# Kernel optimization log

Measured on AMD Instinct MI355X. Metric: run time of the kernel, lower is better.

Reference implementation:

```python
import jax, jax.numpy as jnp
import numpy as np
from jax import lax

WIN = 8
SHIFT = 4
HEADS = 8
EPS = 1e-5

def _rel_pos_index(ws):
    coords = np.stack(np.meshgrid(np.arange(ws), np.arange(ws), indexing='ij'))  # (2,ws,ws)
    flat = coords.reshape(2, -1)
    rel = (flat[:, :, None] - flat[:, None, :]).transpose(1, 2, 0)
    rel[..., 0] += ws - 1
    rel[..., 1] += ws - 1
    rel[..., 0] *= 2 * ws - 1
    return rel.sum(-1)  # (ws*ws, ws*ws)

REL_IDX = _rel_pos_index(WIN)

def _attn_mask(H, W, ws, ss):
    # static shifted-window mask, values 0 / -100 like the torch code
    img = np.zeros((H, W))
    cnt = 0
    for h in (slice(0, -ws), slice(-ws, -ss), slice(-ss, None)):
        for w in (slice(0, -ws), slice(-ws, -ss), slice(-ss, None)):
            img[h, w] = cnt
            cnt += 1
    mw = img.reshape(H // ws, ws, W // ws, ws).transpose(0, 2, 1, 3).reshape(-1, ws * ws)
    diff = mw[:, None, :] - mw[:, :, None]  # [nW,1,N]-[nW,N,1]
    return jnp.asarray(np.where(diff != 0, -100.0, 0.0).astype(np.float32))

def _ln(x, w, b):
    m = x.mean(-1, keepdims=True)
    v = ((x - m) ** 2).mean(-1, keepdims=True)
    return (x - m) / jnp.sqrt(v + EPS) * w + b

def _win_part(x, ws):
    B, H, W, C = x.shape
    x = x.reshape(B, H // ws, ws, W // ws, ws, C).transpose(0, 1, 3, 2, 4, 5)
    return x.reshape(-1, ws * ws, C)

def _win_rev(w, ws, H, W, B):
    x = w.reshape(B, H // ws, W // ws, ws, ws, -1).transpose(0, 1, 3, 2, 4, 5)
    return x.reshape(B, H, W, -1)

def setup_inputs() -> dict:
    key = jax.random.key(0)
    ks = jax.random.split(key, 10)
    B, H, W, C, HID = 4, 128, 128, 256, 1024
    p = lambda i, shape: jax.random.normal(ks[i], shape, jnp.float32) * 0.02
    return dict(
        x=jax.random.normal(ks[0], (B, H * W, C), jnp.float32),
        H=H, W=W,
        norm1_w=jnp.ones((C,), jnp.float32), norm1_b=jnp.zeros((C,), jnp.float32),
        wq=p(1, (C, C)), bq=jnp.zeros((C,), jnp.float32),
        wkv=p(2, (C, 2 * C)), bkv=jnp.zeros((2 * C,), jnp.float32),
        rpb=p(3, ((2 * WIN - 1) ** 2, HEADS)),
        proj_w=p(4, (C, C)), proj_b=jnp.zeros((C,), jnp.float32),
        norm2_w=jnp.ones((C,), jnp.float32), norm2_b=jnp.zeros((C,), jnp.float32),
        lin1_w=p(5, (C, HID)), lin1_b=jnp.zeros((HID,), jnp.float32),
        dw_w=p(6, (HID, 1, 3, 3)), dw_b=jnp.zeros((HID,), jnp.float32),
        lin2_w=p(7, (HID, C)), lin2_b=jnp.zeros((C,), jnp.float32),
    )

def _forward(x, H, W, norm1_w, norm1_b, wq, bq, wkv, bkv, rpb, proj_w, proj_b,
             norm2_w, norm2_b, lin1_w, lin1_b, dw_w, dw_b, lin2_w, lin2_b):
    B, L, C = x.shape
    hd = C // HEADS
    scale = hd ** -0.5
    shortcut = x
    # norm1 + shifted window partition
    xn = _ln(x, norm1_w, norm1_b).reshape(B, H, W, C)
    xs = jnp.roll(xn, (-SHIFT, -SHIFT), axis=(1, 2))
    win = _win_part(xs, WIN)                                # (B*nW, N, C)
    Bw, N, _ = win.shape
    # windowed attention with relative position bias + shift mask
    q = (win @ wq + bq).reshape(Bw, N, HEADS, hd).transpose(0, 2, 1, 3)
    kv = (win @ wkv + bkv).reshape(Bw, N, 2, HEADS, hd).transpose(2, 0, 3, 1, 4)
    k, v = kv[0], kv[1]
    attn = jnp.einsum('bhnd,bhmd->bhnm', q * scale, k)
    bias = rpb[REL_IDX.reshape(-1)].reshape(N, N, HEADS).transpose(2, 0, 1)
    attn = attn + bias[None]
    mask = _attn_mask(H, W, WIN, SHIFT)                      # (nW, N, N)
    nW = mask.shape[0]
    attn = attn.reshape(B, nW, HEADS, N, N) + mask[None, :, None]
    attn = jax.nn.softmax(attn.reshape(Bw, HEADS, N, N), axis=-1)
    o = jnp.einsum('bhnm,bhmd->bhnd', attn, v).transpose(0, 2, 1, 3).reshape(Bw, N, C)
    o = o @ proj_w + proj_b
    # reverse windows + unshift, residual
    xr = _win_rev(o.reshape(-1, WIN, WIN, C), WIN, H, W, B)
    xr = jnp.roll(xr, (SHIFT, SHIFT), axis=(1, 2)).reshape(B, L, C)
    x = shortcut + xr
    # DWCFF: linear -> GELU -> depthwise 3x3 conv -> GELU -> linear, residual
    x2 = _ln(x, norm2_w, norm2_b)
    h = jax.nn.gelu(x2 @ lin1_w + lin1_b, approximate=False)
    HID = h.shape[-1]
    h = h.reshape(B, H, W, HID).transpose(0, 3, 1, 2)        # NCHW
    h = lax.conv_general_dilated(h, dw_w, (1, 1), 'SAME', feature_group_count=HID)
    h = jax.nn.gelu(h + dw_b[None, :, None, None], approximate=False)
    h = h.transpose(0, 2, 3, 1).reshape(B, L, HID)
    return x + (h @ lin2_w + lin2_b)

def reference(x, H, W, norm1_w, norm1_b, wq, bq, wkv, bkv, rpb, proj_w, proj_b,
              norm2_w, norm2_b, lin1_w, lin1_b, dw_w, dw_b, lin2_w, lin2_b):
    return _forward(x, H, W, norm1_w, norm1_b, wq, bq, wkv, bkv, rpb, proj_w,
                    proj_b, norm2_w, norm2_b, lin1_w, lin1_b, dw_w, dw_b,
                    lin2_w, lin2_b)
```

## Files before the change

kernel.cpp:

```cpp
#include <hip/hip_runtime.h>
#include <math.h>


#define TOK   65536
#define CDIM  256
#define HIDD  1024
#define PIXB  16384

typedef __attribute__((ext_vector_type(8))) short bf16x8;
typedef __attribute__((ext_vector_type(4))) float f32x4;

__device__ __forceinline__ float gelu_exact(float v) {
    return 0.5f * v * (1.0f + erff(v * 0.7071067811865476f));
}

__device__ __forceinline__ unsigned short bf16_rne(float f) {
    unsigned u = __float_as_uint(f);
    unsigned r = u + 0x7fffu + ((u >> 16) & 1u);
    return (unsigned short)(r >> 16);
}

__device__ __forceinline__ int win_row_map(int t) {
    int bw = t >> 6, n = t & 63;
    int b = bw >> 8, widx = bw & 255;
    int wh = widx >> 4, ww = widx & 15;
    int i = n >> 3, j = n & 7;
    int h = (wh * 8 + i + 4) & 127;
    int w = (ww * 8 + j + 4) & 127;
    return (b << 14) | (h << 7) | w;
}

template<bool WINDOW>
__global__ __launch_bounds__(256) void ln_kernel(const float* __restrict__ in,
    const float* __restrict__ gw, const float* __restrict__ gb,
    float* __restrict__ out)
{
    int wave = threadIdx.x >> 6;
    int lane = threadIdx.x & 63;
    int t = blockIdx.x * 4 + wave;
    int src = WINDOW ? win_row_map(t) : t;
    const float4 v = *(const float4*)(in + (size_t)src * CDIM + lane * 4);
    float sum = v.x + v.y + v.z + v.w;
    float sq  = v.x * v.x + v.y * v.y + v.z * v.z + v.w * v.w;
#pragma unroll
    for (int off = 32; off > 0; off >>= 1) {
        sum += __shfl_xor(sum, off);
        sq  += __shfl_xor(sq, off);
    }
    float mean = sum * (1.0f / CDIM);
    float var  = sq * (1.0f / CDIM) - mean * mean;
    float rstd = rsqrtf(var + 1e-5f);
    const float4 w4 = *(const float4*)(gw + lane * 4);
    const float4 b4 = *(const float4*)(gb + lane * 4);
    float4 o4;
    o4.x = (v.x - mean) * rstd * w4.x + b4.x;
    o4.y = (v.y - mean) * rstd * w4.y + b4.y;
    o4.z = (v.z - mean) * rstd * w4.z + b4.z;
    o4.w = (v.w - mean) * rstd * w4.w + b4.w;
    *(float4*)(out + (size_t)t * CDIM + lane * 4) = o4;
}

__global__ __launch_bounds__(256) void wprep_kernel(const float* __restrict__ W,
    short* __restrict__ hi, short* __restrict__ lo, int K, int N)
{
    int idx = blockIdx.x * 256 + threadIdx.x;
    if (idx >= K * N) return;
    int k = idx / N, n = idx - k * N;
    float f = W[idx];
    unsigned short h = bf16_rne(f);
    float fh = __uint_as_float((unsigned)h << 16);
    unsigned short l = bf16_rne(f - fh);
    hi[(size_t)n * K + k] = (short)h;
    lo[(size_t)n * K + k] = (short)l;
}

#define EPI_NONE   0
#define EPI_GELU   1
#define EPI_WINRES 2
#define EPI_RES    3

template<int EPI>
__global__ __launch_bounds__(256) void mgemm_kernel(const float* __restrict__ A,
    const short* __restrict__ BTh, const short* __restrict__ BTl,
    const float* __restrict__ bias, float* __restrict__ C,
    const float* __restrict__ R, int M, int N, int K)
{
    __shared__ short lds[4 * 5120];
    short* Ah = lds;
    short* Al = lds + 5120;
    short* Bh = lds + 10240;
    short* Bl = lds + 15360;

    const int tid = threadIdx.x;
    const int bm = blockIdx.y << 7, bn = blockIdx.x << 7;
    const int sr = tid >> 1;
    const int sc = (tid & 1) << 4;

    const float* Aptr = A + (size_t)(bm + sr) * K + sc;
    const short* BhP = BTh + (size_t)(bn + sr) * K + sc;
    const short* BlP = BTl + (size_t)(bn + sr) * K + sc;

    const int wid = tid >> 6, lane = tid & 63;
    const int wr = wid >> 1, wc = wid & 1;
    const int lr = lane & 15, lkq = lane >> 4;
    const int lk = lkq << 3;

    f32x4 acc[4][4] = {};

    for (int k0 = 0; k0 < K; k0 += 32) {
        float va[16];
#pragma unroll
        for (int j = 0; j < 4; ++j) {
            float4 t = *(const float4*)(Aptr + k0 + 4 * j);
            va[4*j+0] = t.x; va[4*j+1] = t.y; va[4*j+2] = t.z; va[4*j+3] = t.w;
        }
        bf16x8 gb0 = *(const bf16x8*)(BhP + k0);
        bf16x8 gb1 = *(const bf16x8*)(BhP + k0 + 8);
        bf16x8 gc0 = *(const bf16x8*)(BlP + k0);
        bf16x8 gc1 = *(const bf16x8*)(BlP + k0 + 8);
        bf16x8 ah0, ah1, al0, al1;
#pragma unroll
        for (int j = 0; j < 8; ++j) {
            unsigned short h0 = bf16_rne(va[j]);
            ah0[j] = (short)h0;
            al0[j] = (short)bf16_rne(va[j] - __uint_as_float((unsigned)h0 << 16));
            unsigned short h1 = bf16_rne(va[j + 8]);
            ah1[j] = (short)h1;
            al1[j] = (short)bf16_rne(va[j + 8] - __uint_as_float((unsigned)h1 << 16));
        }
        __syncthreads();
        *(bf16x8*)&Ah[sr * 40 + sc]     = ah0;
        *(bf16x8*)&Ah[sr * 40 + sc + 8] = ah1;
        *(bf16x8*)&Al[sr * 40 + sc]     = al0;
        *(bf16x8*)&Al[sr * 40 + sc + 8] = al1;
        *(bf16x8*)&Bh[sr * 40 + sc]     = gb0;
        *(bf16x8*)&Bh[sr * 40 + sc + 8] = gb1;
        *(bf16x8*)&Bl[sr * 40 + sc]     = gc0;
        *(bf16x8*)&Bl[sr * 40 + sc + 8] = gc1;
        __syncthreads();

        bf16x8 fah[4], fal[4], fbh[4], fbl[4];
#pragma unroll
        for (int mi = 0; mi < 4; ++mi) {
            int off = (wr * 64 + mi * 16 + lr) * 40 + lk;
            fah[mi] = *(const bf16x8*)&Ah[off];
            fal[mi] = *(const bf16x8*)&Al[off];
        }
#pragma unroll
        for (int ni = 0; ni < 4; ++ni) {
            int off = (wc * 64 + ni * 16 + lr) * 40 + lk;
            fbh[ni] = *(const bf16x8*)&Bh[off];
            fbl[ni] = *(const bf16x8*)&Bl[off];
        }
#pragma unroll
        for (int mi = 0; mi < 4; ++mi)
#pragma unroll
            for (int ni = 0; ni < 4; ++ni) {
                acc[mi][ni] = __builtin_amdgcn_mfma_f32_16x16x32_bf16(
                    fah[mi], fbh[ni], acc[mi][ni], 0, 0, 0);
                acc[mi][ni] = __builtin_amdgcn_mfma_f32_16x16x32_bf16(
                    fah[mi], fbl[ni], acc[mi][ni], 0, 0, 0);
                acc[mi][ni] = __builtin_amdgcn_mfma_f32_16x16x32_bf16(
                    fal[mi], fbh[ni], acc[mi][ni], 0, 0, 0);
            }
    }

#pragma unroll
    for (int mi = 0; mi < 4; ++mi) {
#pragma unroll
        for (int ni = 0; ni < 4; ++ni) {
            int col = bn + wc * 64 + ni * 16 + lr;
            float bv = bias[col];
#pragma unroll
            for (int r = 0; r < 4; ++r) {
                int row = bm + wr * 64 + mi * 16 + lkq * 4 + r;
                float v = acc[mi][ni][r] + bv;
                if (EPI == EPI_GELU) v = gelu_exact(v);
                int drow = (EPI == EPI_WINRES) ? win_row_map(row) : row;
                if (EPI == EPI_WINRES || EPI == EPI_RES)
                    v += R[(size_t)drow * N + col];
                C[(size_t)drow * N + col] = v;
            }
        }
    }
}

__global__ __launch_bounds__(64) void attn_kernel(float* __restrict__ q,
    const float* __restrict__ kv, const float* __restrict__ rpb)
{
    __shared__ float kS[64][32];
    __shared__ float vS[64][32];
    int blk = blockIdx.x;
    int bw = blk >> 3, head = blk & 7;
    int lane = threadIdx.x;

    size_t kvrow = ((size_t)(bw * 64 + lane)) * 512 + head * 32;
#pragma unroll
    for (int d0 = 0; d0 < 8; ++d0) {
        *(float4*)(&kS[lane][d0 * 4]) = *(const float4*)(kv + kvrow + d0 * 4);
        *(float4*)(&vS[lane][d0 * 4]) = *(const float4*)(kv + kvrow + 256 + d0 * 4);
    }
    float4 qr[8];
    size_t qrow = ((size_t)(bw * 64 + lane)) * 256 + head * 32;
#pragma unroll
    for (int d0 = 0; d0 < 8; ++d0)
        qr[d0] = *(const float4*)(q + qrow + d0 * 4);
    __syncthreads();

    int widx = bw & 255;
    int wh = widx >> 4, ww = widx & 15;
    int i1 = lane >> 3, j1 = lane & 7;
    int h1 = wh * 8 + i1, w1 = ww * 8 + j1;
    int lbl1 = (h1 < 120 ? 0 : (h1 < 124 ? 1 : 2)) * 3
             + (w1 < 120 ? 0 : (w1 < 124 ? 1 : 2));
    const float scale = 0.17677669529663687f;

    float s[64];
    float mx = -1e30f;
#pragma unroll
    for (int m = 0; m < 64; ++m) {
        float a = 0.f;
#pragma unroll
        for (int d0 = 0; d0 < 8; ++d0) {
            float4 kk = *(const float4*)(&kS[m][d0 * 4]);
            a = fmaf(qr[d0].x, kk.x, a);
            a = fmaf(qr[d0].y, kk.y, a);
            a = fmaf(qr[d0].z, kk.z, a);
            a = fmaf(qr[d0].w, kk.w, a);
        }
        int i2 = m >> 3, j2 = m & 7;
        int idx = (i1 - i2 + 7) * 15 + (j1 - j2 + 7);
        float b = rpb[idx * 8 + head];
        int h2 = wh * 8 + i2, w2 = ww * 8 + j2;
        int lbl2 = (h2 < 120 ? 0 : (h2 < 124 ? 1 : 2)) * 3
                 + (w2 < 120 ? 0 : (w2 < 124 ? 1 : 2));
        float sv = a * scale + b + ((lbl1 != lbl2) ? -100.f : 0.f);
        s[m] = sv;
        mx = fmaxf(mx, sv);
    }
    float sum = 0.f;
#pragma unroll
    for (int m = 0; m < 64; ++m) {
        float e = __expf(s[m] - mx);
        s[m] = e;
        sum += e;
    }
    float inv = 1.0f / sum;

    float oa[32];
#pragma unroll
    for (int d = 0; d < 32; ++d) oa[d] = 0.f;
#pragma unroll
    for (int m = 0; m < 64; ++m) {
        float p = s[m];
#pragma unroll
        for (int d0 = 0; d0 < 8; ++d0) {
            float4 vv = *(const float4*)(&vS[m][d0 * 4]);
            oa[d0 * 4 + 0] = fmaf(p, vv.x, oa[d0 * 4 + 0]);
            oa[d0 * 4 + 1] = fmaf(p, vv.y, oa[d0 * 4 + 1]);
            oa[d0 * 4 + 2] = fmaf(p, vv.z, oa[d0 * 4 + 2]);
            oa[d0 * 4 + 3] = fmaf(p, vv.w, oa[d0 * 4 + 3]);
        }
    }
#pragma unroll
    for (int d0 = 0; d0 < 8; ++d0) {
        float4 ov = make_float4(oa[d0 * 4 + 0] * inv, oa[d0 * 4 + 1] * inv,
                                oa[d0 * 4 + 2] * inv, oa[d0 * 4 + 3] * inv);
        *(float4*)(q + qrow + d0 * 4) = ov;
    }
}

__global__ __launch_bounds__(256) void prep_dw_kernel(const float* __restrict__ dww,
    float* __restrict__ wT)
{
    int gid = blockIdx.x * 256 + threadIdx.x;
    if (gid >= 9 * HIDD) return;
    int k = gid >> 10, c = gid & 1023;
    wT[gid] = dww[c * 9 + k];
}

__global__ __launch_bounds__(256) void dwconv_kernel(const float* __restrict__ h,
    const float* __restrict__ wT, const float* __restrict__ db,
    float* __restrict__ out, int y0)
{
    int gid = blockIdx.x * 256 + threadIdx.x;
    int c = (gid & 255) << 2;
    int pix = gid >> 8;
    int x = pix & 127, y = y0 + (pix >> 7);

    float4 acc = *(const float4*)(db + c);
#pragma unroll
    for (int ky = 0; ky < 3; ++ky) {
        int yy = y + ky - 1;
        if (yy < 0 || yy > 127) continue;
#pragma unroll
        for (int kx = 0; kx < 3; ++kx) {
            int xx = x + kx - 1;
            if (xx < 0 || xx > 127) continue;
            float4 iv = *(const float4*)(h + ((size_t)((yy << 7) | xx) << 10) + c);
            float4 wv = *(const float4*)(wT + (ky * 3 + kx) * HIDD + c);
            acc.x = fmaf(iv.x, wv.x, acc.x);
            acc.y = fmaf(iv.y, wv.y, acc.y);
            acc.z = fmaf(iv.z, wv.z, acc.z);
            acc.w = fmaf(iv.w, wv.w, acc.w);
        }
    }
    float4 o4 = make_float4(gelu_exact(acc.x), gelu_exact(acc.y),
                            gelu_exact(acc.z), gelu_exact(acc.w));
    *(float4*)(out + ((size_t)pix << 10) + c) = o4;
}

extern "C" void kernel_launch(void* const* d_in, const int* in_sizes, int n_in,
                              void* d_out, int out_size, void* d_ws, size_t ws_size,
                              hipStream_t stream) {
    const float* x    = (const float*)d_in[0];
    const float* n1w  = (const float*)d_in[3];
    const float* n1b  = (const float*)d_in[4];
    const float* wq   = (const float*)d_in[5];
    const float* bq   = (const float*)d_in[6];
    const float* wkv  = (const float*)d_in[7];
    const float* bkv  = (const float*)d_in[8];
    const float* rpb  = (const float*)d_in[9];
    const float* pw   = (const float*)d_in[10];
    const float* pb   = (const float*)d_in[11];
    const float* n2w  = (const float*)d_in[12];
    const float* n2b  = (const float*)d_in[13];
    const float* l1w  = (const float*)d_in[14];
    const float* l1b  = (const float*)d_in[15];
    const float* dww  = (const float*)d_in[16];
    const float* dwb  = (const float*)d_in[17];
    const float* l2w  = (const float*)d_in[18];
    const float* l2b  = (const float*)d_in[19];
    float* out = (float*)d_out;
    float* ws  = (float*)d_ws;

    const size_t MC = (size_t)TOK * CDIM;
    const size_t BC = (size_t)PIXB * CDIM;
    float* wT    = ws;
    short* WThi  = (short*)(ws + 16384);
    short* WTlo  = (short*)(ws + 16384 + 393216);
    float* base  = ws + 1048576;
    float* win   = out;
    float* x1    = out;

    const size_t OQ = 0, OKV = 65536, OP = 196608, OL1 = 262144, OL2 = 524288;

    const bool full = ws_size >= (1048576 + 3 * MC) * sizeof(float);

    ln_kernel<true><<<TOK / 4, 256, 0, stream>>>(x, n1w, n1b, win);
    prep_dw_kernel<<<(9 * HIDD + 255) / 256, 256, 0, stream>>>(dww, wT);
    wprep_kernel<<<(256 * 256 + 255) / 256, 256, 0, stream>>>(wq,  WThi + OQ,  WTlo + OQ,  256, 256);
    wprep_kernel<<<(256 * 512 + 255) / 256, 256, 0, stream>>>(wkv, WThi + OKV, WTlo + OKV, 256, 512);
    wprep_kernel<<<(256 * 256 + 255) / 256, 256, 0, stream>>>(pw,  WThi + OP,  WTlo + OP,  256, 256);
    wprep_kernel<<<(256 * 1024 + 255) / 256, 256, 0, stream>>>(l1w, WThi + OL1, WTlo + OL1, 256, 1024);
    wprep_kernel<<<(1024 * 256 + 255) / 256, 256, 0, stream>>>(l2w, WThi + OL2, WTlo + OL2, 1024, 256);

    if (full) {
        float* qb  = base;
        float* x2  = base;
        float* kvb = base + MC;
        float* hbB = base + MC;
        float* hcB = base + 2 * MC;

        mgemm_kernel<EPI_NONE><<<dim3(2, TOK / 128), 256, 0, stream>>>(
            win, WThi + OQ, WTlo + OQ, bq, qb, nullptr, TOK, CDIM, CDIM);
        mgemm_kernel<EPI_NONE><<<dim3(4, TOK / 128), 256, 0, stream>>>(
            win, WThi + OKV, WTlo + OKV, bkv, kvb, nullptr, TOK, 2 * CDIM, CDIM);
        attn_kernel<<<(TOK / 64) * 8, 64, 0, stream>>>(qb, kvb, rpb);
        mgemm_kernel<EPI_WINRES><<<dim3(2, TOK / 128), 256, 0, stream>>>(
            qb, WThi + OP, WTlo + OP, pb, x1, x, TOK, CDIM, CDIM);
        ln_kernel<false><<<TOK / 4, 256, 0, stream>>>(x1, n2w, n2b, x2);
        for (int b = 0; b < 4; ++b) {
            const float* x2b = x2 + (size_t)b * BC;
            const float* x1b = x1 + (size_t)b * BC;
            float* outb = out + (size_t)b * BC;
            mgemm_kernel<EPI_GELU><<<dim3(8, PIXB / 128), 256, 0, stream>>>(
                x2b, WThi + OL1, WTlo + OL1, l1b, hbB, nullptr, PIXB, HIDD, CDIM);
            dwconv_kernel<<<PIXB * (HIDD / 4) / 256, 256, 0, stream>>>(
                hbB, wT, dwb, hcB, 0);
            mgemm_kernel<EPI_RES><<<dim3(2, PIXB / 128), 256, 0, stream>>>(
                hcB, WThi + OL2, WTlo + OL2, l2b, outb, x1b, PIXB, CDIM, HIDD);
        }
    } else {
        float* qb_s  = base;
        float* kvb_s = base + MC / 4;
        for (int b = 0; b < 4; ++b) {
            const float* winb = win + (size_t)b * BC;
            const float* xb   = x   + (size_t)b * BC;
            float* x1b = x1 + (size_t)b * BC;
            mgemm_kernel<EPI_NONE><<<dim3(2, PIXB / 128), 256, 0, stream>>>(
                winb, WThi + OQ, WTlo + OQ, bq, qb_s, nullptr, PIXB, CDIM, CDIM);
            mgemm_kernel<EPI_NONE><<<dim3(4, PIXB / 128), 256, 0, stream>>>(
                winb, WThi + OKV, WTlo + OKV, bkv, kvb_s, nullptr, PIXB, 2 * CDIM, CDIM);
            attn_kernel<<<(PIXB / 64) * 8, 64, 0, stream>>>(qb_s, kvb_s, rpb);
            mgemm_kernel<EPI_WINRES><<<dim3(2, PIXB / 128), 256, 0, stream>>>(
                qb_s, WThi + OP, WTlo + OP, pb, x1b, xb, PIXB, CDIM, CDIM);
        }
        float* x2_s = base;
        float* hb_s = base + MC / 4;
        float* hc_s = base + MC / 4 + MC;
        const int SROWS = 32, SPIX = SROWS * 128;
        for (int b = 0; b < 4; ++b) {
            const float* x1b = x1 + (size_t)b * BC;
            float* outb = out + (size_t)b * BC;
            ln_kernel<false><<<PIXB / 4, 256, 0, stream>>>(x1b, n2w, n2b, x2_s);
            mgemm_kernel<EPI_GELU><<<dim3(8, PIXB / 128), 256, 0, stream>>>(
                x2_s, WThi + OL1, WTlo + OL1, l1b, hb_s, nullptr, PIXB, HIDD, CDIM);
            for (int s = 0; s < 4; ++s) {
                dwconv_kernel<<<SPIX * (HIDD / 4) / 256, 256, 0, stream>>>(
                    hb_s, wT, dwb, hc_s, s * SROWS);
                mgemm_kernel<EPI_RES><<<dim3(2, SPIX / 128), 256, 0, stream>>>(
                    hc_s, WThi + OL2, WTlo + OL2, l2b,
                    outb + (size_t)s * SPIX * CDIM,
                    x1b + (size_t)s * SPIX * CDIM, SPIX, CDIM, HIDD);
            }
        }
    }
}
```

Measured before the change: 1.159 ms.

## Store activations as pre-split bf16 hi/lo pairs and prefetch GEMM tiles

Producers (layernorms, QKV GEMMs, attention, depthwise conv) now write activations as split bf16 hi/lo arrays, so the GEMMs load ready-made operands instead of converting fp32 inside the K loop. The GEMM gains a register prefetch of the next K tile. Attention switches to an online softmax, reads a precomputed bias table, and evaluates the shift mask only for boundary windows. The reduced-workspace fallback path is removed, which adds a workspace size requirement and keeps the same two-bf16 precision scheme.

```diff
diff --git a/kernel.cpp b/kernel.cpp
--- a/kernel.cpp
+++ b/kernel.cpp
@@ -8,16 +8,27 @@
 #define PIXB  16384
 
 typedef __attribute__((ext_vector_type(8))) short bf16x8;
+typedef __attribute__((ext_vector_type(4))) short s16x4;
 typedef __attribute__((ext_vector_type(4))) float f32x4;
 
 __device__ __forceinline__ float gelu_exact(float v) {
     return 0.5f * v * (1.0f + erff(v * 0.7071067811865476f));
 }
-
 __device__ __forceinline__ unsigned short bf16_rne(float f) {
     unsigned u = __float_as_uint(f);
     unsigned r = u + 0x7fffu + ((u >> 16) & 1u);
     return (unsigned short)(r >> 16);
+}
+__device__ __forceinline__ float bf16_f(short s) {
+    return __uint_as_float(((unsigned)(unsigned short)s) << 16);
+}
+struct HL { short h, l; };
+__device__ __forceinline__ HL split2(float f) {
+    HL r;
+    unsigned short uh = bf16_rne(f);
+    r.h = (short)uh;
+    r.l = (short)bf16_rne(f - __uint_as_float((unsigned)uh << 16));
+    return r;
 }
 
 __device__ __forceinline__ int win_row_map(int t) {
@@ -33,7 +44,7 @@
 template<bool WINDOW>
 __global__ __launch_bounds__(256) void ln_kernel(const float* __restrict__ in,
     const float* __restrict__ gw, const float* __restrict__ gb,
-    float* __restrict__ out)
+    short* __restrict__ oh, short* __restrict__ ol)
 {
     int wave = threadIdx.x >> 6;
     int lane = threadIdx.x & 63;
@@ -52,12 +63,18 @@
     float rstd = rsqrtf(var + 1e-5f);
     const float4 w4 = *(const float4*)(gw + lane * 4);
     const float4 b4 = *(const float4*)(gb + lane * 4);
-    float4 o4;
-    o4.x = (v.x - mean) * rstd * w4.x + b4.x;
-    o4.y = (v.y - mean) * rstd * w4.y + b4.y;
-    o4.z = (v.z - mean) * rstd * w4.z + b4.z;
-    o4.w = (v.w - mean) * rstd * w4.w + b4.w;
-    *(float4*)(out + (size_t)t * CDIM + lane * 4) = o4;
+    float o0 = (v.x - mean) * rstd * w4.x + b4.x;
+    float o1 = (v.y - mean) * rstd * w4.y + b4.y;
+    float o2 = (v.z - mean) * rstd * w4.z + b4.z;
+    float o3 = (v.w - mean) * rstd * w4.w + b4.w;
+    s16x4 vh, vl;
+    HL r0 = split2(o0); vh[0] = r0.h; vl[0] = r0.l;
+    HL r1 = split2(o1); vh[1] = r1.h; vl[1] = r1.l;
+    HL r2 = split2(o2); vh[2] = r2.h; vl[2] = r2.l;
+    HL r3 = split2(o3); vh[3] = r3.h; vl[3] = r3.l;
+    size_t o = (size_t)t * CDIM + lane * 4;
+    *(s16x4*)(oh + o) = vh;
+    *(s16x4*)(ol + o) = vl;
 }
 
 __global__ __launch_bounds__(256) void wprep_kernel(const float* __restrict__ W,
@@ -66,24 +83,35 @@
     int idx = blockIdx.x * 256 + threadIdx.x;
     if (idx >= K * N) return;
     int k = idx / N, n = idx - k * N;
-    float f = W[idx];
-    unsigned short h = bf16_rne(f);
-    float fh = __uint_as_float((unsigned)h << 16);
-    unsigned short l = bf16_rne(f - fh);
-    hi[(size_t)n * K + k] = (short)h;
-    lo[(size_t)n * K + k] = (short)l;
-}
-
-#define EPI_NONE   0
+    HL r = split2(W[idx]);
+    hi[(size_t)n * K + k] = r.h;
+    lo[(size_t)n * K + k] = r.l;
+}
+
+__global__ __launch_bounds__(256) void bias_prep_kernel(
+    const float* __restrict__ rpb, float* __restrict__ bias8T)
+{
+    int gid = blockIdx.x * 256 + threadIdx.x;
+    if (gid >= 8 * 64 * 64) return;
+    int h = gid >> 12, m = (gid >> 6) & 63, q = gid & 63;
+    int qi = q >> 3, qj = q & 7, mi = m >> 3, mj = m & 7;
+    int ridx = (qi - mi + 7) * 15 + (qj - mj + 7);
+    bias8T[gid] = rpb[ridx * 8 + h];
+}
+
+#define EPI_PAIR   0
 #define EPI_GELU   1
 #define EPI_WINRES 2
 #define EPI_RES    3
 
 template<int EPI>
-__global__ __launch_bounds__(256) void mgemm_kernel(const float* __restrict__ A,
+__global__ __launch_bounds__(256) void mgemm_kernel(
+    const short* __restrict__ Agh, const short* __restrict__ Agl,
     const short* __restrict__ BTh, const short* __restrict__ BTl,
-    const float* __restrict__ bias, float* __restrict__ C,
-    const float* __restrict__ R, int M, int N, int K)
+    const float* __restrict__ bias,
+    float* __restrict__ C, const float* __restrict__ R,
+    short* __restrict__ Ch, short* __restrict__ Cl,
+    int M, int N, int K)
 {
     __shared__ short lds[4 * 5120];
     short* Ah = lds;
@@ -96,9 +124,10 @@
     const int sr = tid >> 1;
     const int sc = (tid & 1) << 4;
 
-    const float* Aptr = A + (size_t)(bm + sr) * K + sc;
-    const short* BhP = BTh + (size_t)(bn + sr) * K + sc;
-    const short* BlP = BTl + (size_t)(bn + sr) * K + sc;
+    const short* pAh = Agh + (size_t)(bm + sr) * K + sc;
+    const short* pAl = Agl + (size_t)(bm + sr) * K + sc;
+    const short* pBh = BTh + (size_t)(bn + sr) * K + sc;
+    const short* pBl = BTl + (size_t)(bn + sr) * K + sc;
 
     const int wid = tid >> 6, lane = tid & 63;
     const int wr = wid >> 1, wc = wid & 1;
@@ -107,37 +136,36 @@
 
     f32x4 acc[4][4] = {};
 
+    bf16x8 rah0 = *(const bf16x8*)(pAh);
+    bf16x8 rah1 = *(const bf16x8*)(pAh + 8);
+    bf16x8 ral0 = *(const bf16x8*)(pAl);
+    bf16x8 ral1 = *(const bf16x8*)(pAl + 8);
+    bf16x8 rbh0 = *(const bf16x8*)(pBh);
+    bf16x8 rbh1 = *(const bf16x8*)(pBh + 8);
+    bf16x8 rbl0 = *(const bf16x8*)(pBl);
+    bf16x8 rbl1 = *(const bf16x8*)(pBl + 8);
+
     for (int k0 = 0; k0 < K; k0 += 32) {
-        float va[16];
-#pragma unroll
-        for (int j = 0; j < 4; ++j) {
-            float4 t = *(const float4*)(Aptr + k0 + 4 * j);
-            va[4*j+0] = t.x; va[4*j+1] = t.y; va[4*j+2] = t.z; va[4*j+3] = t.w;
-        }
-        bf16x8 gb0 = *(const bf16x8*)(BhP + k0);
-        bf16x8 gb1 = *(const bf16x8*)(BhP + k0 + 8);
-        bf16x8 gc0 = *(const bf16x8*)(BlP + k0);
-        bf16x8 gc1 = *(const bf16x8*)(BlP + k0 + 8);
-        bf16x8 ah0, ah1, al0, al1;
-#pragma unroll
-        for (int j = 0; j < 8; ++j) {
-            unsigned short h0 = bf16_rne(va[j]);
-            ah0[j] = (short)h0;
-            al0[j] = (short)bf16_rne(va[j] - __uint_as_float((unsigned)h0 << 16));
-            unsigned short h1 = bf16_rne(va[j + 8]);
-            ah1[j] = (short)h1;
-            al1[j] = (short)bf16_rne(va[j + 8] - __uint_as_float((unsigned)h1 << 16));
-        }
         __syncthreads();
-        *(bf16x8*)&Ah[sr * 40 + sc]     = ah0;
-        *(bf16x8*)&Ah[sr * 40 + sc + 8] = ah1;
-        *(bf16x8*)&Al[sr * 40 + sc]     = al0;
-        *(bf16x8*)&Al[sr * 40 + sc + 8] = al1;
-        *(bf16x8*)&Bh[sr * 40 + sc]     = gb0;
-        *(bf16x8*)&Bh[sr * 40 + sc + 8] = gb1;
-        *(bf16x8*)&Bl[sr * 40 + sc]     = gc0;
-        *(bf16x8*)&Bl[sr * 40 + sc + 8] = gc1;
+        *(bf16x8*)&Ah[sr * 40 + sc]     = rah0;
+        *(bf16x8*)&Ah[sr * 40 + sc + 8] = rah1;
+        *(bf16x8*)&Al[sr * 40 + sc]     = ral0;
+        *(bf16x8*)&Al[sr * 40 + sc + 8] = ral1;
+        *(bf16x8*)&Bh[sr * 40 + sc]     = rbh0;
+        *(bf16x8*)&Bh[sr * 40 + sc + 8] = rbh1;
+        *(bf16x8*)&Bl[sr * 40 + sc]     = rbl0;
+        *(bf16x8*)&Bl[sr * 40 + sc + 8] = rbl1;
         __syncthreads();
+        if (k0 + 32 < K) {
+            rah0 = *(const bf16x8*)(pAh + k0 + 32);
+            rah1 = *(const bf16x8*)(pAh + k0 + 40);
+            ral0 = *(const bf16x8*)(pAl + k0 + 32);
+            ral1 = *(const bf16x8*)(pAl + k0 + 40);
+            rbh0 = *(const bf16x8*)(pBh + k0 + 32);
+            rbh1 = *(const bf16x8*)(pBh + k0 + 40);
+            rbl0 = *(const bf16x8*)(pBl + k0 + 32);
+            rbl1 = *(const bf16x8*)(pBl + k0 + 40);
+        }
 
         bf16x8 fah[4], fal[4], fbh[4], fbl[4];
 #pragma unroll
@@ -179,94 +207,106 @@
                 int drow = (EPI == EPI_WINRES) ? win_row_map(row) : row;
                 if (EPI == EPI_WINRES || EPI == EPI_RES)
                     v += R[(size_t)drow * N + col];
-                C[(size_t)drow * N + col] = v;
+                if (EPI == EPI_PAIR) {
+                    HL s = split2(v);
+                    Ch[(size_t)row * N + col] = s.h;
+                    Cl[(size_t)row * N + col] = s.l;
+                } else {
+                    C[(size_t)drow * N + col] = v;
+                }
             }
         }
     }
 }
 
-__global__ __launch_bounds__(64) void attn_kernel(float* __restrict__ q,
-    const float* __restrict__ kv, const float* __restrict__ rpb)
-{
-    __shared__ float kS[64][32];
-    __shared__ float vS[64][32];
+__global__ __launch_bounds__(64) void attn_kernel(
+    short* __restrict__ qh, short* __restrict__ ql,
+    const short* __restrict__ kvh, const short* __restrict__ kvl,
+    const float* __restrict__ bias8T)
+{
+    __shared__ float kS[64][33];
+    __shared__ float vS[64][33];
     int blk = blockIdx.x;
     int bw = blk >> 3, head = blk & 7;
     int lane = threadIdx.x;
 
-    size_t kvrow = ((size_t)(bw * 64 + lane)) * 512 + head * 32;
-#pragma unroll
-    for (int d0 = 0; d0 < 8; ++d0) {
-        *(float4*)(&kS[lane][d0 * 4]) = *(const float4*)(kv + kvrow + d0 * 4);
-        *(float4*)(&vS[lane][d0 * 4]) = *(const float4*)(kv + kvrow + 256 + d0 * 4);
-    }
-    float4 qr[8];
-    size_t qrow = ((size_t)(bw * 64 + lane)) * 256 + head * 32;
-#pragma unroll
-    for (int d0 = 0; d0 < 8; ++d0)
-        qr[d0] = *(const float4*)(q + qrow + d0 * 4);
+    size_t ekv = ((size_t)(bw * 64 + lane)) * 512 + head * 32;
+#pragma unroll
+    for (int j = 0; j < 4; ++j) {
+        bf16x8 h8 = *(const bf16x8*)(kvh + ekv + j * 8);
+        bf16x8 l8 = *(const bf16x8*)(kvl + ekv + j * 8);
+#pragma unroll
+        for (int e = 0; e < 8; ++e)
+            kS[lane][j * 8 + e] = bf16_f(h8[e]) + bf16_f(l8[e]);
+        bf16x8 hv = *(const bf16x8*)(kvh + ekv + 256 + j * 8);
+        bf16x8 lv = *(const bf16x8*)(kvl + ekv + 256 + j * 8);
+#pragma unroll
+        for (int e = 0; e < 8; ++e)
+            vS[lane][j * 8 + e] = bf16_f(hv[e]) + bf16_f(lv[e]);
+    }
+    float qr[32];
+    size_t eq = ((size_t)(bw * 64 + lane)) * 256 + head * 32;
+#pragma unroll
+    for (int j = 0; j < 4; ++j) {
+        bf16x8 h8 = *(const bf16x8*)(qh + eq + j * 8);
+        bf16x8 l8 = *(const bf16x8*)(ql + eq + j * 8);
+#pragma unroll
+        for (int e = 0; e < 8; ++e)
+            qr[j * 8 + e] = bf16_f(h8[e]) + bf16_f(l8[e]);
+    }
     __syncthreads();
 
     int widx = bw & 255;
     int wh = widx >> 4, ww = widx & 15;
+    const bool boundary = (wh == 15) || (ww == 15);
     int i1 = lane >> 3, j1 = lane & 7;
     int h1 = wh * 8 + i1, w1 = ww * 8 + j1;
     int lbl1 = (h1 < 120 ? 0 : (h1 < 124 ? 1 : 2)) * 3
              + (w1 < 120 ? 0 : (w1 < 124 ? 1 : 2));
     const float scale = 0.17677669529663687f;
-
-    float s[64];
-    float mx = -1e30f;
-#pragma unroll
+    const float* bT = bias8T + head * 4096;
+
+    float mx = -1e30f, sum = 0.f;
+    float oa[32];
+#pragma unroll
+    for (int d = 0; d < 32; ++d) oa[d] = 0.f;
+
     for (int m = 0; m < 64; ++m) {
         float a = 0.f;
 #pragma unroll
-        for (int d0 = 0; d0 < 8; ++d0) {
-            float4 kk = *(const float4*)(&kS[m][d0 * 4]);
-            a = fmaf(qr[d0].x, kk.x, a);
-            a = fmaf(qr[d0].y, kk.y, a);
-            a = fmaf(qr[d0].z, kk.z, a);
-            a = fmaf(qr[d0].w, kk.w, a);
-        }
-        int i2 = m >> 3, j2 = m & 7;
-        int idx = (i1 - i2 + 7) * 15 + (j1 - j2 + 7);
-        float b = rpb[idx * 8 + head];
-        int h2 = wh * 8 + i2, w2 = ww * 8 + j2;
-        int lbl2 = (h2 < 120 ? 0 : (h2 < 124 ? 1 : 2)) * 3
-                 + (w2 < 120 ? 0 : (w2 < 124 ? 1 : 2));
-        float sv = a * scale + b + ((lbl1 != lbl2) ? -100.f : 0.f);
-        s[m] = sv;
-        mx = fmaxf(mx, sv);
-    }
-    float sum = 0.f;
-#pragma unroll
-    for (int m = 0; m < 64; ++m) {
-        float e = __expf(s[m] - mx);
-        s[m] = e;
+        for (int d = 0; d < 32; ++d) a = fmaf(qr[d], kS[m][d], a);
+        float sv = a * scale + bT[m * 64 + lane];
+        if (boundary) {
+            int i2 = m >> 3, j2 = m & 7;
+            int h2 = wh * 8 + i2, w2 = ww * 8 + j2;
+            int lbl2 = (h2 < 120 ? 0 : (h2 < 124 ? 1 : 2)) * 3
+                     + (w2 < 120 ? 0 : (w2 < 124 ? 1 : 2));
+            if (lbl1 != lbl2) sv -= 100.f;
+        }
+        if (sv > mx) {
+            float r = __expf(mx - sv);
+            sum *= r;
+#pragma unroll
+            for (int d = 0; d < 32; ++d) oa[d] *= r;
+            mx = sv;
+        }
+        float e = __expf(sv - mx);
         sum += e;
-    }
+#pragma unroll
+        for (int d = 0; d < 32; ++d) oa[d] = fmaf(e, vS[m][d], oa[d]);
+    }
+
     float inv = 1.0f / sum;
-
-    float oa[32];
-#pragma unroll
-    for (int d = 0; d < 32; ++d) oa[d] = 0.f;
-#pragma unroll
-    for (int m = 0; m < 64; ++m) {
-        float p = s[m];
-#pragma unroll
-        for (int d0 = 0; d0 < 8; ++d0) {
-            float4 vv = *(const float4*)(&vS[m][d0 * 4]);
-            oa[d0 * 4 + 0] = fmaf(p, vv.x, oa[d0 * 4 + 0]);
-            oa[d0 * 4 + 1] = fmaf(p, vv.y, oa[d0 * 4 + 1]);
-            oa[d0 * 4 + 2] = fmaf(p, vv.z, oa[d0 * 4 + 2]);
-            oa[d0 * 4 + 3] = fmaf(p, vv.w, oa[d0 * 4 + 3]);
-        }
-    }
-#pragma unroll
-    for (int d0 = 0; d0 < 8; ++d0) {
-        float4 ov = make_float4(oa[d0 * 4 + 0] * inv, oa[d0 * 4 + 1] * inv,
-                                oa[d0 * 4 + 2] * inv, oa[d0 * 4 + 3] * inv);
-        *(float4*)(q + qrow + d0 * 4) = ov;
+#pragma unroll
+    for (int j = 0; j < 4; ++j) {
+        bf16x8 vh, vl;
+#pragma unroll
+        for (int e = 0; e < 8; ++e) {
+            HL s = split2(oa[j * 8 + e] * inv);
+            vh[e] = s.h; vl[e] = s.l;
+        }
+        *(bf16x8*)(qh + eq + j * 8) = vh;
+        *(bf16x8*)(ql + eq + j * 8) = vl;
     }
 }
 
@@ -281,12 +321,12 @@
 
 __global__ __launch_bounds__(256) void dwconv_kernel(const float* __restrict__ h,
     const float* __restrict__ wT, const float* __restrict__ db,
-    float* __restrict__ out, int y0)
+    short* __restrict__ oh, short* __restrict__ ol)
 {
     int gid = blockIdx.x * 256 + threadIdx.x;
     int c = (gid & 255) << 2;
     int pix = gid >> 8;
-    int x = pix & 127, y = y0 + (pix >> 7);
+    int x = pix & 127, y = pix >> 7;
 
     float4 acc = *(const float4*)(db + c);
 #pragma unroll
@@ -305,9 +345,14 @@
             acc.w = fmaf(iv.w, wv.w, acc.w);
         }
     }
-    float4 o4 = make_float4(gelu_exact(acc.x), gelu_exact(acc.y),
-                            gelu_exact(acc.z), gelu_exact(acc.w));
-    *(float4*)(out + ((size_t)pix << 10) + c) = o4;
+    s16x4 vh, vl;
+    HL r0 = split2(gelu_exact(acc.x)); vh[0] = r0.h; vl[0] = r0.l;
+    HL r1 = split2(gelu_exact(acc.y)); vh[1] = r1.h; vl[1] = r1.l;
+    HL r2 = split2(gelu_exact(acc.z)); vh[2] = r2.h; vl[2] = r2.l;
+    HL r3 = split2(gelu_exact(acc.w)); vh[3] = r3.h; vl[3] = r3.l;
+    size_t o = ((size_t)pix << 10) + c;
+    *(s16x4*)(oh + o) = vh;
+    *(s16x4*)(ol + o) = vl;
 }
 
 extern "C" void kernel_launch(void* const* d_in, const int* in_sizes, int n_in,
@@ -336,84 +381,62 @@
 
     const size_t MC = (size_t)TOK * CDIM;
     const size_t BC = (size_t)PIXB * CDIM;
-    float* wT    = ws;
-    short* WThi  = (short*)(ws + 16384);
-    short* WTlo  = (short*)(ws + 16384 + 393216);
-    float* base  = ws + 1048576;
-    float* win   = out;
-    float* x1    = out;
+
+    float* wT     = ws;
+    short* WThi   = (short*)(ws + 16384);
+    short* WTlo   = (short*)(ws + 16384 + 393216);
+    float* bias8T = ws + 802816;
+    float* base   = ws + 1048576;
+
+    short* sbase = (short*)base;
+    short* qh  = sbase;
+    short* ql  = sbase + MC;
+    short* x2h = sbase;
+    short* x2l = sbase + MC;
+    short* kvh = sbase + 2 * MC;
+    short* kvl = sbase + 4 * MC;
+    float* hb  = base + MC;
+    short* hch = (short*)(base + 2 * MC);
+    short* hcl = hch + MC;
+
+    short* winh = (short*)out;
+    short* winl = winh + MC;
+    float* x1   = out;
 
     const size_t OQ = 0, OKV = 65536, OP = 196608, OL1 = 262144, OL2 = 524288;
 
-    const bool full = ws_size >= (1048576 + 3 * MC) * sizeof(float);
-
-    ln_kernel<true><<<TOK / 4, 256, 0, stream>>>(x, n1w, n1b, win);
+    ln_kernel<true><<<TOK / 4, 256, 0, stream>>>(x, n1w, n1b, winh, winl);
     prep_dw_kernel<<<(9 * HIDD + 255) / 256, 256, 0, stream>>>(dww, wT);
+    bias_prep_kernel<<<(8 * 64 * 64) / 256, 256, 0, stream>>>(rpb, bias8T);
     wprep_kernel<<<(256 * 256 + 255) / 256, 256, 0, stream>>>(wq,  WThi + OQ,  WTlo + OQ,  256, 256);
     wprep_kernel<<<(256 * 512 + 255) / 256, 256, 0, stream>>>(wkv, WThi + OKV, WTlo + OKV, 256, 512);
     wprep_kernel<<<(256 * 256 + 255) / 256, 256, 0, stream>>>(pw,  WThi + OP,  WTlo + OP,  256, 256);
     wprep_kernel<<<(256 * 1024 + 255) / 256, 256, 0, stream>>>(l1w, WThi + OL1, WTlo + OL1, 256, 1024);
     wprep_kernel<<<(1024 * 256 + 255) / 256, 256, 0, stream>>>(l2w, WThi + OL2, WTlo + OL2, 1024, 256);
 
-    if (full) {
-        float* qb  = base;
-        float* x2  = base;
-        float* kvb = base + MC;
-        float* hbB = base + MC;
-        float* hcB = base + 2 * MC;
-
-        mgemm_kernel<EPI_NONE><<<dim3(2, TOK / 128), 256, 0, stream>>>(
-            win, WThi + OQ, WTlo + OQ, bq, qb, nullptr, TOK, CDIM, CDIM);
-        mgemm_kernel<EPI_NONE><<<dim3(4, TOK / 128), 256, 0, stream>>>(
-            win, WThi + OKV, WTlo + OKV, bkv, kvb, nullptr, TOK, 2 * CDIM, CDIM);
-        attn_kernel<<<(TOK / 64) * 8, 64, 0, stream>>>(qb, kvb, rpb);
-        mgemm_kernel<EPI_WINRES><<<dim3(2, TOK / 128), 256, 0, stream>>>(
-            qb, WThi + OP, WTlo + OP, pb, x1, x, TOK, CDIM, CDIM);
-        ln_kernel<false><<<TOK / 4, 256, 0, stream>>>(x1, n2w, n2b, x2);
-        for (int b = 0; b < 4; ++b) {
-            const float* x2b = x2 + (size_t)b * BC;
-            const float* x1b = x1 + (size_t)b * BC;
-            float* outb = out + (size_t)b * BC;
-            mgemm_kernel<EPI_GELU><<<dim3(8, PIXB / 128), 256, 0, stream>>>(
-                x2b, WThi + OL1, WTlo + OL1, l1b, hbB, nullptr, PIXB, HIDD, CDIM);
-            dwconv_kernel<<<PIXB * (HIDD / 4) / 256, 256, 0, stream>>>(
-                hbB, wT, dwb, hcB, 0);
-            mgemm_kernel<EPI_RES><<<dim3(2, PIXB / 128), 256, 0, stream>>>(
-                hcB, WThi + OL2, WTlo + OL2, l2b, outb, x1b, PIXB, CDIM, HIDD);
-        }
-    } else {
-        float* qb_s  = base;
-        float* kvb_s = base + MC / 4;
-        for (int b = 0; b < 4; ++b) {
-            const float* winb = win + (size_t)b * BC;
-            const float* xb   = x   + (size_t)b * BC;
-            float* x1b = x1 + (size_t)b * BC;
-            mgemm_kernel<EPI_NONE><<<dim3(2, PIXB / 128), 256, 0, stream>>>(
-                winb, WThi + OQ, WTlo + OQ, bq, qb_s, nullptr, PIXB, CDIM, CDIM);
-            mgemm_kernel<EPI_NONE><<<dim3(4, PIXB / 128), 256, 0, stream>>>(
-                winb, WThi + OKV, WTlo + OKV, bkv, kvb_s, nullptr, PIXB, 2 * CDIM, CDIM);
-            attn_kernel<<<(PIXB / 64) * 8, 64, 0, stream>>>(qb_s, kvb_s, rpb);
-            mgemm_kernel<EPI_WINRES><<<dim3(2, PIXB / 128), 256, 0, stream>>>(
-                qb_s, WThi + OP, WTlo + OP, pb, x1b, xb, PIXB, CDIM, CDIM);
-        }
-        float* x2_s = base;
-        float* hb_s = base + MC / 4;
-        float* hc_s = base + MC / 4 + MC;
-        const int SROWS = 32, SPIX = SROWS * 128;
-        for (int b = 0; b < 4; ++b) {
-            const float* x1b = x1 + (size_t)b * BC;
-            float* outb = out + (size_t)b * BC;
-            ln_kernel<false><<<PIXB / 4, 256, 0, stream>>>(x1b, n2w, n2b, x2_s);
-            mgemm_kernel<EPI_GELU><<<dim3(8, PIXB / 128), 256, 0, stream>>>(
-                x2_s, WThi + OL1, WTlo + OL1, l1b, hb_s, nullptr, PIXB, HIDD, CDIM);
-            for (int s = 0; s < 4; ++s) {
-                dwconv_kernel<<<SPIX * (HIDD / 4) / 256, 256, 0, stream>>>(
-                    hb_s, wT, dwb, hc_s, s * SROWS);
-                mgemm_kernel<EPI_RES><<<dim3(2, SPIX / 128), 256, 0, stream>>>(
-                    hc_s, WThi + OL2, WTlo + OL2, l2b,
-                    outb + (size_t)s * SPIX * CDIM,
-                    x1b + (size_t)s * SPIX * CDIM, SPIX, CDIM, HIDD);
-            }
-        }
-    }
-}
+    mgemm_kernel<EPI_PAIR><<<dim3(2, TOK / 128), 256, 0, stream>>>(
+        winh, winl, WThi + OQ, WTlo + OQ, bq, nullptr, nullptr, qh, ql,
+        TOK, CDIM, CDIM);
+    mgemm_kernel<EPI_PAIR><<<dim3(4, TOK / 128), 256, 0, stream>>>(
+        winh, winl, WThi + OKV, WTlo + OKV, bkv, nullptr, nullptr, kvh, kvl,
+        TOK, 2 * CDIM, CDIM);
+    attn_kernel<<<(TOK / 64) * 8, 64, 0, stream>>>(qh, ql, kvh, kvl, bias8T);
+    mgemm_kernel<EPI_WINRES><<<dim3(2, TOK / 128), 256, 0, stream>>>(
+        qh, ql, WThi + OP, WTlo + OP, pb, x1, x, nullptr, nullptr,
+        TOK, CDIM, CDIM);
+    ln_kernel<false><<<TOK / 4, 256, 0, stream>>>(x1, n2w, n2b, x2h, x2l);
+    for (int b = 0; b < 4; ++b) {
+        const short* x2hb = x2h + (size_t)b * BC;
+        const short* x2lb = x2l + (size_t)b * BC;
+        const float* x1b  = x1 + (size_t)b * BC;
+        float* outb = out + (size_t)b * BC;
+        mgemm_kernel<EPI_GELU><<<dim3(8, PIXB / 128), 256, 0, stream>>>(
+            (const short*)x2hb, (const short*)x2lb, WThi + OL1, WTlo + OL1,
+            l1b, hb, nullptr, nullptr, nullptr, PIXB, HIDD, CDIM);
+        dwconv_kernel<<<PIXB * (HIDD / 4) / 256, 256, 0, stream>>>(
+            hb, wT, dwb, hch, hcl);
+        mgemm_kernel<EPI_RES><<<dim3(2, PIXB / 128), 256, 0, stream>>>(
+            hch, hcl, WThi + OL2, WTlo + OL2, l2b, outb, x1b, nullptr, nullptr,
+            PIXB, CDIM, HIDD);
+    }
+}
```

Result: faster. 1.135 ms (-2.1%).
